# Kernel optimization log

Measured on AMD Instinct MI355X. Metric: run time of the kernel, lower is better.

Reference implementation:

```python
import jax, jax.numpy as jnp
import numpy as np

SCALE = 8.0  # sqrt(d_k), d_k = 64
NEG_INF = -1000000000.0


def setup_inputs() -> dict:
    key = jax.random.key(0)
    ks = jax.random.split(key, 7)
    B, H, S, D = 2, 8, 4096, 64
    shp = (B, H, S, D)
    q_a = jax.random.normal(ks[0], shp, dtype=jnp.float32)
    k_a = jax.random.normal(ks[1], shp, dtype=jnp.float32)
    v_a = jax.random.normal(ks[2], shp, dtype=jnp.float32)
    q_s = jax.random.normal(ks[3], shp, dtype=jnp.float32)
    k_s = jax.random.normal(ks[4], shp, dtype=jnp.float32)
    v_s = jax.random.normal(ks[5], shp, dtype=jnp.float32)
    mask = jax.random.randint(ks[6], (B, 1, 1, S), 0, 2, dtype=jnp.int32)
    return {"q_a": q_a, "k_a": k_a, "v_a": v_a,
            "q_s": q_s, "k_s": k_s, "v_s": v_s, "mask": mask}


def reference(q_a, k_a, v_a, q_s, k_s, v_s, mask):
    # a2a + a2s + s2a + s2s == (q_a + q_s) @ (k_a + k_s)^T  (exact algebra)
    q = q_a + q_s                               # [B,H,S,D]
    k = k_a + k_s                               # [B,H,S,D]
    score = jnp.einsum("bhqd,bhkd->bhqk", q, k) / SCALE  # [B,H,S,S]
    score = jnp.where(mask == 0, NEG_INF, score)
    attn = jax.nn.softmax(score, axis=-1)       # dropout p=0 (eval/identity)
    out = jnp.einsum("bhqk,bhkd->bhqd", attn, v_a + v_s)
    return out
```

## Files before the change

### kernel.cpp

```cpp
#include <hip/hip_runtime.h>
#include <hip/hip_bf16.h>

#define S_   4096
#define D_   64
#define BH_  16
#define QW   64
#define QBLK 256
#define KVB  128
#define NCH  2

typedef __attribute__((ext_vector_type(8)))  short short8_t;
typedef __attribute__((ext_vector_type(16))) float f32x16;
#define QSCALE 0.18033688011112042f

__device__ __forceinline__ unsigned short f2bf(float f) {
  unsigned u = __float_as_uint(f);
  u += 0x7fffu + ((u >> 16) & 1u);
  return (unsigned short)(u >> 16);
}

__device__ __forceinline__ void glds16(const unsigned short* g, unsigned short* l) {
  __builtin_amdgcn_global_load_lds(
      (const __attribute__((address_space(1))) unsigned int*)g,
      (__attribute__((address_space(3))) unsigned int*)l, 16, 0, 0);
}

__global__ void addcvt2_kernel(const float* __restrict__ a, const float* __restrict__ b,
                               unsigned short* __restrict__ o, float scale, int n) {
  int i = (blockIdx.x * blockDim.x + threadIdx.x) * 4;
  if (i >= n) return;
  float4 x = *(const float4*)(a + i);
  float4 y = *(const float4*)(b + i);
  ushort4 r;
  r.x = f2bf((x.x + y.x) * scale); r.y = f2bf((x.y + y.y) * scale);
  r.z = f2bf((x.z + y.z) * scale); r.w = f2bf((x.w + y.w) * scale);
  *(ushort4*)(o + i) = r;
}

__global__ void compact_kernel(const int* __restrict__ mask, int* __restrict__ idx,
                               int* __restrict__ cnt) {
  __shared__ int ps[256];
  int b = blockIdx.x, tid = threadIdx.x;
  const int* mb = mask + (size_t)b * S_;
  int m[16], c = 0;
  int base = tid * 16;
#pragma unroll
  for (int i = 0; i < 16; ++i) { m[i] = mb[base + i]; c += (m[i] != 0); }
  ps[tid] = c;
  __syncthreads();
  for (int off = 1; off < 256; off <<= 1) {
    int add = (tid >= off) ? ps[tid - off] : 0;
    __syncthreads();
    ps[tid] += add;
    __syncthreads();
  }
  int pos = ps[tid] - c;
#pragma unroll
  for (int i = 0; i < 16; ++i) if (m[i]) idx[(size_t)b * S_ + pos++] = base + i;
  if (tid == 255) cnt[b] = ps[255];
}

__global__ void kgather_kernel(const float* __restrict__ ka, const float* __restrict__ ks,
                               const int* __restrict__ idx, const int* __restrict__ cnt,
                               unsigned short* __restrict__ khat) {
  int gid = blockIdx.x * 256 + threadIdx.x;
  int e = gid * 8;
  int bh = e >> 18;
  int rem = e & 262143;
  int j = rem >> 6, d = rem & 63;
  int b = bh >> 3;
  int C = cnt[b];
  unsigned short* o = khat + (size_t)e;
  ushort4 r0 = {0, 0, 0, 0}, r1 = {0, 0, 0, 0};
  if (j < C) {
    int src = idx[(size_t)b * S_ + j];
    const float* pa = ka + ((size_t)bh * S_ + src) * D_ + d;
    const float* pb = ks + ((size_t)bh * S_ + src) * D_ + d;
    float4 x0 = *(const float4*)pa, x1 = *(const float4*)(pa + 4);
    float4 y0 = *(const float4*)pb, y1 = *(const float4*)(pb + 4);
    r0.x = f2bf(x0.x + y0.x); r0.y = f2bf(x0.y + y0.y);
    r0.z = f2bf(x0.z + y0.z); r0.w = f2bf(x0.w + y0.w);
    r1.x = f2bf(x1.x + y1.x); r1.y = f2bf(x1.y + y1.y);
    r1.z = f2bf(x1.z + y1.z); r1.w = f2bf(x1.w + y1.w);
  }
  *(ushort4*)o = r0;
  *(ushort4*)(o + 4) = r1;
}

__global__ void vgather_kernel(const float* __restrict__ va, const float* __restrict__ vs,
                               const int* __restrict__ idx, const int* __restrict__ cnt,
                               unsigned short* __restrict__ vt) {
  __shared__ __align__(16) unsigned short t[D_][72];
  int bh = blockIdx.y, b = bh >> 3;
  int s0 = blockIdx.x * 64;
  int C = cnt[b];
  int tid = threadIdx.x;
  int row16 = tid >> 4;
  int col4  = (tid & 15) * 4;
#pragma unroll
  for (int p = 0; p < 4; ++p) {
    int srow = p * 16 + row16;
    int j = s0 + srow;
    float4 x = {0, 0, 0, 0}, y = {0, 0, 0, 0};
    if (j < C) {
      int src = idx[(size_t)b * S_ + j];
      x = *(const float4*)(va + ((size_t)bh * S_ + src) * D_ + col4);
      y = *(const float4*)(vs + ((size_t)bh * S_ + src) * D_ + col4);
    }
    t[col4 + 0][srow] = f2bf(x.x + y.x);
    t[col4 + 1][srow] = f2bf(x.y + y.y);
    t[col4 + 2][srow] = f2bf(x.z + y.z);
    t[col4 + 3][srow] = f2bf(x.w + y.w);
  }
  __syncthreads();
#pragma unroll
  for (int r = 0; r < 2; ++r) {
    int e = (r * 256 + tid) * 8;
    int d = e >> 6, sc = e & 63;
    short8_t v = *(const short8_t*)&t[d][sc];
    *(short8_t*)(vt + ((size_t)bh * D_ + d) * S_ + s0 + sc) = v;
  }
}

__global__ __launch_bounds__(256, 2) void attn_kernel(
    const unsigned short* __restrict__ Qb, const unsigned short* __restrict__ Kb,
    const unsigned short* __restrict__ Vt, const int* __restrict__ cnt,
    float* __restrict__ out, float* __restrict__ Opar, float2* __restrict__ Ml) {
  __shared__ __align__(16) unsigned short lK[2][KVB * 64];
  __shared__ __align__(16) unsigned short lV[2][64 * KVB];

  const int tid  = threadIdx.x;
  const int wave = tid >> 6;
  const int lane = tid & 63;
  const int l31  = lane & 31;
  const int h5   = lane >> 5;
  const int rsw  = l31 & 7;
  const int bh   = blockIdx.y;
  const int ch   = blockIdx.z;
  const int qrow0 = blockIdx.x * QBLK + wave * QW + l31;
  const int b    = bh >> 3;
  const int C    = cnt[b];
  const int NTt  = (C + KVB - 1) / KVB;
  const int tpc  = (NTt + NCH - 1) / NCH;
  const int ts   = ch * tpc;
  const int te   = (ts + tpc < NTt) ? (ts + tpc) : NTt;

  short8_t qf[2][4];
#pragma unroll
  for (int qb = 0; qb < 2; ++qb) {
    const unsigned short* qp = Qb + ((size_t)bh * S_ + qrow0 + 32 * qb) * D_ + h5 * 8;
#pragma unroll
    for (int t4 = 0; t4 < 4; ++t4) qf[qb][t4] = *(const short8_t*)(qp + t4 * 16);
  }

  const unsigned short* gk0 = Kb + (size_t)bh * S_ * D_;
  const unsigned short* gv0 = Vt + (size_t)bh * D_ * S_;

  int srcK[4], srcV[4], ldsB[4];
#pragma unroll
  for (int r2 = 0; r2 < 4; ++r2) {
    int c = r2 * 256 + tid;
    int rowK = c >> 3, gK = (c & 7) ^ (rowK & 7);
    srcK[r2] = rowK * 64 + gK * 8;
    int rowV = c >> 4, gg = c & 15;
    int swg = (gg & 8) | ((gg & 7) ^ (rowV & 7));
    srcV[r2] = rowV * S_ + swg * 8;
    ldsB[r2] = r2 * 2048 + wave * 512;
  }

  f32x16 acc0[2], acc1[2];
  float mrow[2], lrow[2];
#pragma unroll
  for (int qb = 0; qb < 2; ++qb) {
    acc0[qb] = (f32x16)(0.0f); acc1[qb] = (f32x16)(0.0f);
    mrow[qb] = -1e30f; lrow[qb] = 0.0f;
  }

  if (ts < te) {
#pragma unroll
    for (int r2 = 0; r2 < 4; ++r2) {
      glds16(gk0 + (size_t)ts * KVB * D_ + srcK[r2], &lK[0][ldsB[r2]]);
      glds16(gv0 + ts * KVB + srcV[r2], &lV[0][ldsB[r2]]);
    }
    __syncthreads();

    for (int t = ts; t < te; ++t) {
      const int cur = (t - ts) & 1;
      if (t + 1 < te) {
#pragma unroll
        for (int r2 = 0; r2 < 4; ++r2) {
          glds16(gk0 + (size_t)(t + 1) * KVB * D_ + srcK[r2], &lK[cur ^ 1][ldsB[r2]]);
          glds16(gv0 + (t + 1) * KVB + srcV[r2], &lV[cur ^ 1][ldsB[r2]]);
        }
      }

#pragma unroll
      for (int h = 0; h < 2; ++h) {
        f32x16 sv0[2], sv1[2];
#pragma unroll
        for (int qb = 0; qb < 2; ++qb) { sv0[qb] = (f32x16)(0.0f); sv1[qb] = (f32x16)(0.0f); }
        __builtin_amdgcn_s_setprio(1);
#pragma unroll
        for (int t4 = 0; t4 < 4; ++t4) {
          int g = ((2 * t4 + h5) ^ rsw) * 8;
          short8_t kf0 = *(const short8_t*)&lK[cur][(h * 64 + l31) * 64 + g];
          short8_t kf1 = *(const short8_t*)&lK[cur][(h * 64 + 32 + l31) * 64 + g];
          sv0[0] = __builtin_amdgcn_mfma_f32_32x32x16_bf16(kf0, qf[0][t4], sv0[0], 0, 0, 0);
          sv0[1] = __builtin_amdgcn_mfma_f32_32x32x16_bf16(kf0, qf[1][t4], sv0[1], 0, 0, 0);
          sv1[0] = __builtin_amdgcn_mfma_f32_32x32x16_bf16(kf1, qf[0][t4], sv1[0], 0, 0, 0);
          sv1[1] = __builtin_amdgcn_mfma_f32_32x32x16_bf16(kf1, qf[1][t4], sv1[1], 0, 0, 0);
        }
        __builtin_amdgcn_s_setprio(0);

        if (t == NTt - 1) {
          int kvb = t * KVB + h * 64;
#pragma unroll
          for (int i = 0; i < 16; ++i) {
            int key = kvb + (i & 3) + 8 * (i >> 2) + 4 * h5;
#pragma unroll
            for (int qb = 0; qb < 2; ++qb) {
              if (key >= C) sv0[qb][i] = -1e9f;
              if (key + 32 >= C) sv1[qb][i] = -1e9f;
            }
          }
        }

        unsigned int pkw[2][16];
#pragma unroll
        for (int qb = 0; qb < 2; ++qb) {
          float tmx[8];
#pragma unroll
          for (int i = 0; i < 8; ++i)
            tmx[i] = fmaxf(fmaxf(sv0[qb][i], sv0[qb][i + 8]),
                           fmaxf(sv1[qb][i], sv1[qb][i + 8]));
#pragma unroll
          for (int i = 0; i < 4; ++i) tmx[i] = fmaxf(tmx[i], tmx[i + 4]);
          float tm = fmaxf(fmaxf(tmx[0], tmx[1]), fmaxf(tmx[2], tmx[3]));
          tm = fmaxf(tm, __shfl_xor(tm, 32));

          if (__any(tm > mrow[qb] + 8.0f)) {
            float mnew = fmaxf(mrow[qb], tm);
            float sc = __builtin_amdgcn_exp2f(mrow[qb] - mnew);
            mrow[qb] = mnew;
            lrow[qb] *= sc;
#pragma unroll
            for (int i = 0; i < 16; ++i) { acc0[qb][i] *= sc; acc1[qb][i] *= sc; }
          }

          float m = mrow[qb];
          float t0 = 0.f, t1 = 0.f, t2 = 0.f, t3 = 0.f;
#pragma unroll
          for (int i = 0; i < 16; i += 4) {
            sv0[qb][i + 0] = __builtin_amdgcn_exp2f(sv0[qb][i + 0] - m); t0 += sv0[qb][i + 0];
            sv0[qb][i + 1] = __builtin_amdgcn_exp2f(sv0[qb][i + 1] - m); t1 += sv0[qb][i + 1];
            sv0[qb][i + 2] = __builtin_amdgcn_exp2f(sv0[qb][i + 2] - m); t2 += sv0[qb][i + 2];
            sv0[qb][i + 3] = __builtin_amdgcn_exp2f(sv0[qb][i + 3] - m); t3 += sv0[qb][i + 3];
            sv1[qb][i + 0] = __builtin_amdgcn_exp2f(sv1[qb][i + 0] - m); t0 += sv1[qb][i + 0];
            sv1[qb][i + 1] = __builtin_amdgcn_exp2f(sv1[qb][i + 1] - m); t1 += sv1[qb][i + 1];
            sv1[qb][i + 2] = __builtin_amdgcn_exp2f(sv1[qb][i + 2] - m); t2 += sv1[qb][i + 2];
            sv1[qb][i + 3] = __builtin_amdgcn_exp2f(sv1[qb][i + 3] - m); t3 += sv1[qb][i + 3];
          }
          float tsum = (t0 + t1) + (t2 + t3);
          tsum += __shfl_xor(tsum, 32);
          lrow[qb] += tsum;

#pragma unroll
          for (int rg = 0; rg < 4; ++rg) {
            __hip_bfloat162 a0 = __float22bfloat162_rn({sv0[qb][rg * 4 + 0], sv0[qb][rg * 4 + 1]});
            __hip_bfloat162 a1 = __float22bfloat162_rn({sv0[qb][rg * 4 + 2], sv0[qb][rg * 4 + 3]});
            __hip_bfloat162 b0 = __float22bfloat162_rn({sv1[qb][rg * 4 + 0], sv1[qb][rg * 4 + 1]});
            __hip_bfloat162 b1 = __float22bfloat162_rn({sv1[qb][rg * 4 + 2], sv1[qb][rg * 4 + 3]});
            pkw[qb][rg * 2 + 0] = *(unsigned int*)&a0;
            pkw[qb][rg * 2 + 1] = *(unsigned int*)&a1;
            pkw[qb][8 + rg * 2 + 0] = *(unsigned int*)&b0;
            pkw[qb][8 + rg * 2 + 1] = *(unsigned int*)&b1;
          }
        }

        __builtin_amdgcn_s_setprio(1);
#pragma unroll
        for (int kt = 0; kt < 4; ++kt) {
          const int n = kt >> 1, k1 = kt & 1;
          int gcol = ((h * 8) | ((2 * kt + h5) ^ rsw)) * 8;
          short8_t vf0 = *(const short8_t*)&lV[cur][l31 * KVB + gcol];
          short8_t vf1 = *(const short8_t*)&lV[cur][(32 + l31) * KVB + gcol];
#pragma unroll
          for (int qb = 0; qb < 2; ++qb) {
            unsigned int sA = pkw[qb][n * 8 + (2 * k1 + h5) * 2 + 0];
            unsigned int sB = pkw[qb][n * 8 + (2 * k1 + h5) * 2 + 1];
            unsigned int xA = pkw[qb][n * 8 + (2 * k1 + (h5 ^ 1)) * 2 + 0];
            unsigned int xB = pkw[qb][n * 8 + (2 * k1 + (h5 ^ 1)) * 2 + 1];
            unsigned int pA = (unsigned int)__shfl_xor((int)xA, 32);
            unsigned int pB = (unsigned int)__shfl_xor((int)xB, 32);
            union { unsigned int u[4]; short8_t v; } bb;
            bb.u[0] = h5 ? pA : sA;
            bb.u[1] = h5 ? pB : sB;
            bb.u[2] = h5 ? sA : pA;
            bb.u[3] = h5 ? sB : pB;
            acc0[qb] = __builtin_amdgcn_mfma_f32_32x32x16_bf16(vf0, bb.v, acc0[qb], 0, 0, 0);
            acc1[qb] = __builtin_amdgcn_mfma_f32_32x32x16_bf16(vf1, bb.v, acc1[qb], 0, 0, 0);
          }
        }
        __builtin_amdgcn_s_setprio(0);
      }

      __syncthreads();
    }
  }

  float* Op = (ch == 0) ? out : Opar;
#pragma unroll
  for (int qb = 0; qb < 2; ++qb) {
    float* op = Op + ((size_t)bh * S_ + qrow0 + 32 * qb) * D_;
#pragma unroll
    for (int rg = 0; rg < 4; ++rg) {
      float4 o0, o1;
      o0.x = acc0[qb][rg * 4 + 0]; o0.y = acc0[qb][rg * 4 + 1];
      o0.z = acc0[qb][rg * 4 + 2]; o0.w = acc0[qb][rg * 4 + 3];
      o1.x = acc1[qb][rg * 4 + 0]; o1.y = acc1[qb][rg * 4 + 1];
      o1.z = acc1[qb][rg * 4 + 2]; o1.w = acc1[qb][rg * 4 + 3];
      *(float4*)(op + rg * 8 + h5 * 4) = o0;
      *(float4*)(op + 32 + rg * 8 + h5 * 4) = o1;
    }
    if (h5 == 0) {
      float2 st; st.x = mrow[qb]; st.y = lrow[qb];
      Ml[(size_t)ch * (BH_ * S_) + (size_t)bh * S_ + qrow0 + 32 * qb] = st;
    }
  }
}

__global__ void combine_kernel(const float* __restrict__ O1, const float2* __restrict__ Ml,
                               float* __restrict__ out) {
  int gid = blockIdx.x * 256 + threadIdx.x;
  int row = gid >> 2, qd = (gid & 3) * 16;
  float2 a = Ml[row];
  float2 b = Ml[BH_ * S_ + row];
  float M = fmaxf(a.x, b.x);
  float w0 = exp2f(a.x - M), w1 = exp2f(b.x - M);
  float inv = 1.0f / (a.y * w0 + b.y * w1);
  w0 *= inv; w1 *= inv;
  const float4* p0 = (const float4*)(out + (size_t)row * D_ + qd);
  const float4* p1 = (const float4*)(O1 + (size_t)row * D_ + qd);
  float4* po = (float4*)(out + (size_t)row * D_ + qd);
#pragma unroll
  for (int i = 0; i < 4; ++i) {
    float4 x = p0[i], y = p1[i];
    float4 r;
    r.x = x.x * w0 + y.x * w1; r.y = x.y * w0 + y.y * w1;
    r.z = x.z * w0 + y.z * w1; r.w = x.w * w0 + y.w * w1;
    po[i] = r;
  }
}

extern "C" void kernel_launch(void* const* d_in, const int* in_sizes, int n_in,
                              void* d_out, int out_size, void* d_ws, size_t ws_size,
                              hipStream_t stream) {
  const float* q_a = (const float*)d_in[0];
  const float* k_a = (const float*)d_in[1];
  const float* v_a = (const float*)d_in[2];
  const float* q_s = (const float*)d_in[3];
  const float* k_s = (const float*)d_in[4];
  const float* v_s = (const float*)d_in[5];
  const int*   mask = (const int*)d_in[6];
  float* out = (float*)d_out;
  (void)in_sizes; (void)n_in; (void)out_size; (void)ws_size;

  const int N = BH_ * S_ * D_;
  unsigned short* qb   = (unsigned short*)d_ws;
  unsigned short* khat = qb + N;
  unsigned short* vt   = khat + N;
  int*  idx  = (int*)(vt + N);
  int*  cnt  = idx + 2 * S_;
  float* O1  = (float*)(cnt + 4);
  float2* ml = (float2*)(O1 + N);

  compact_kernel<<<2, 256, 0, stream>>>(mask, idx, cnt);
  addcvt2_kernel<<<N / 1024, 256, 0, stream>>>(q_a, q_s, qb, QSCALE, N);
  kgather_kernel<<<N / 2048, 256, 0, stream>>>(k_a, k_s, idx, cnt, khat);
  {
    dim3 g(S_ / 64, BH_);
    vgather_kernel<<<g, 256, 0, stream>>>(v_a, v_s, idx, cnt, vt);
  }
  {
    dim3 g(S_ / QBLK, BH_, NCH);
    attn_kernel<<<g, 256, 0, stream>>>(qb, khat, vt, cnt, out, O1, ml);
  }
  combine_kernel<<<(BH_ * S_ * 4) / 256, 256, 0, stream>>>(O1, ml, out);
}
```

Baseline: 128.7 us.

## Fuse K and V gather kernels and interleave softmax with PV MFMAs per query block

Merges the separate K-gather and V-gather preprocessing kernels into one kernel that reads K and V rows through a single index lookup, saving one launch and a redundant idx read. It also restructures the attention inner loop so that each 32-row query block packs its P values and immediately issues its PV MFMAs, instead of packing both blocks before the MFMA phase. This is meant to shrink the live register set (pkw halves) and let the second block's exp work overlap the first block's matrix ops. The cost is a slightly different instruction schedule, plus K writes done as strided 8-byte stores from the V-transposing tile layout.

```diff
diff --git a/kernel.cpp b/kernel.cpp
--- a/kernel.cpp
+++ b/kernel.cpp
@@ -60,36 +60,11 @@
   if (tid == 255) cnt[b] = ps[255];
 }
 
-__global__ void kgather_kernel(const float* __restrict__ ka, const float* __restrict__ ks,
-                               const int* __restrict__ idx, const int* __restrict__ cnt,
-                               unsigned short* __restrict__ khat) {
-  int gid = blockIdx.x * 256 + threadIdx.x;
-  int e = gid * 8;
-  int bh = e >> 18;
-  int rem = e & 262143;
-  int j = rem >> 6, d = rem & 63;
-  int b = bh >> 3;
-  int C = cnt[b];
-  unsigned short* o = khat + (size_t)e;
-  ushort4 r0 = {0, 0, 0, 0}, r1 = {0, 0, 0, 0};
-  if (j < C) {
-    int src = idx[(size_t)b * S_ + j];
-    const float* pa = ka + ((size_t)bh * S_ + src) * D_ + d;
-    const float* pb = ks + ((size_t)bh * S_ + src) * D_ + d;
-    float4 x0 = *(const float4*)pa, x1 = *(const float4*)(pa + 4);
-    float4 y0 = *(const float4*)pb, y1 = *(const float4*)(pb + 4);
-    r0.x = f2bf(x0.x + y0.x); r0.y = f2bf(x0.y + y0.y);
-    r0.z = f2bf(x0.z + y0.z); r0.w = f2bf(x0.w + y0.w);
-    r1.x = f2bf(x1.x + y1.x); r1.y = f2bf(x1.y + y1.y);
-    r1.z = f2bf(x1.z + y1.z); r1.w = f2bf(x1.w + y1.w);
-  }
-  *(ushort4*)o = r0;
-  *(ushort4*)(o + 4) = r1;
-}
-
-__global__ void vgather_kernel(const float* __restrict__ va, const float* __restrict__ vs,
-                               const int* __restrict__ idx, const int* __restrict__ cnt,
-                               unsigned short* __restrict__ vt) {
+__global__ void kvgather_kernel(const float* __restrict__ ka, const float* __restrict__ ks,
+                                const float* __restrict__ va, const float* __restrict__ vs,
+                                const int* __restrict__ idx, const int* __restrict__ cnt,
+                                unsigned short* __restrict__ khat,
+                                unsigned short* __restrict__ vt) {
   __shared__ __align__(16) unsigned short t[D_][72];
   int bh = blockIdx.y, b = bh >> 3;
   int s0 = blockIdx.x * 64;
@@ -101,16 +76,24 @@
   for (int p = 0; p < 4; ++p) {
     int srow = p * 16 + row16;
     int j = s0 + srow;
-    float4 x = {0, 0, 0, 0}, y = {0, 0, 0, 0};
+    float4 xv = {0, 0, 0, 0}, yv = {0, 0, 0, 0};
+    float4 xk = {0, 0, 0, 0}, yk = {0, 0, 0, 0};
     if (j < C) {
       int src = idx[(size_t)b * S_ + j];
-      x = *(const float4*)(va + ((size_t)bh * S_ + src) * D_ + col4);
-      y = *(const float4*)(vs + ((size_t)bh * S_ + src) * D_ + col4);
-    }
-    t[col4 + 0][srow] = f2bf(x.x + y.x);
-    t[col4 + 1][srow] = f2bf(x.y + y.y);
-    t[col4 + 2][srow] = f2bf(x.z + y.z);
-    t[col4 + 3][srow] = f2bf(x.w + y.w);
+      size_t off = ((size_t)bh * S_ + src) * D_ + col4;
+      xv = *(const float4*)(va + off);
+      yv = *(const float4*)(vs + off);
+      xk = *(const float4*)(ka + off);
+      yk = *(const float4*)(ks + off);
+    }
+    t[col4 + 0][srow] = f2bf(xv.x + yv.x);
+    t[col4 + 1][srow] = f2bf(xv.y + yv.y);
+    t[col4 + 2][srow] = f2bf(xv.z + yv.z);
+    t[col4 + 3][srow] = f2bf(xv.w + yv.w);
+    ushort4 rk;
+    rk.x = f2bf(xk.x + yk.x); rk.y = f2bf(xk.y + yk.y);
+    rk.z = f2bf(xk.z + yk.z); rk.w = f2bf(xk.w + yk.w);
+    *(ushort4*)(khat + ((size_t)bh * S_ + j) * D_ + col4) = rk;
   }
   __syncthreads();
 #pragma unroll
@@ -225,7 +208,6 @@
           }
         }
 
-        unsigned int pkw[2][16];
 #pragma unroll
         for (int qb = 0; qb < 2; ++qb) {
           float tmx[8];
@@ -264,44 +246,49 @@
           tsum += __shfl_xor(tsum, 32);
           lrow[qb] += tsum;
 
+          unsigned int pkw[16];
 #pragma unroll
           for (int rg = 0; rg < 4; ++rg) {
             __hip_bfloat162 a0 = __float22bfloat162_rn({sv0[qb][rg * 4 + 0], sv0[qb][rg * 4 + 1]});
             __hip_bfloat162 a1 = __float22bfloat162_rn({sv0[qb][rg * 4 + 2], sv0[qb][rg * 4 + 3]});
             __hip_bfloat162 b0 = __float22bfloat162_rn({sv1[qb][rg * 4 + 0], sv1[qb][rg * 4 + 1]});
             __hip_bfloat162 b1 = __float22bfloat162_rn({sv1[qb][rg * 4 + 2], sv1[qb][rg * 4 + 3]});
-            pkw[qb][rg * 2 + 0] = *(unsigned int*)&a0;
-            pkw[qb][rg * 2 + 1] = *(unsigned int*)&a1;
-            pkw[qb][8 + rg * 2 + 0] = *(unsigned int*)&b0;
-            pkw[qb][8 + rg * 2 + 1] = *(unsigned int*)&b1;
-          }
-        }
-
-        __builtin_amdgcn_s_setprio(1);
-#pragma unroll
-        for (int kt = 0; kt < 4; ++kt) {
-          const int n = kt >> 1, k1 = kt & 1;
-          int gcol = ((h * 8) | ((2 * kt + h5) ^ rsw)) * 8;
-          short8_t vf0 = *(const short8_t*)&lV[cur][l31 * KVB + gcol];
-          short8_t vf1 = *(const short8_t*)&lV[cur][(32 + l31) * KVB + gcol];
-#pragma unroll
-          for (int qb = 0; qb < 2; ++qb) {
-            unsigned int sA = pkw[qb][n * 8 + (2 * k1 + h5) * 2 + 0];
-            unsigned int sB = pkw[qb][n * 8 + (2 * k1 + h5) * 2 + 1];
-            unsigned int xA = pkw[qb][n * 8 + (2 * k1 + (h5 ^ 1)) * 2 + 0];
-            unsigned int xB = pkw[qb][n * 8 + (2 * k1 + (h5 ^ 1)) * 2 + 1];
+            pkw[rg * 2 + 0] = *(unsigned int*)&a0;
+            pkw[rg * 2 + 1] = *(unsigned int*)&a1;
+            pkw[8 + rg * 2 + 0] = *(unsigned int*)&b0;
+            pkw[8 + rg * 2 + 1] = *(unsigned int*)&b1;
+          }
+
+          unsigned int bbu[4][4];
+#pragma unroll
+          for (int kt = 0; kt < 4; ++kt) {
+            const int n = kt >> 1, k1 = kt & 1;
+            unsigned int sA = pkw[n * 8 + (2 * k1 + h5) * 2 + 0];
+            unsigned int sB = pkw[n * 8 + (2 * k1 + h5) * 2 + 1];
+            unsigned int xA = pkw[n * 8 + (2 * k1 + (h5 ^ 1)) * 2 + 0];
+            unsigned int xB = pkw[n * 8 + (2 * k1 + (h5 ^ 1)) * 2 + 1];
             unsigned int pA = (unsigned int)__shfl_xor((int)xA, 32);
             unsigned int pB = (unsigned int)__shfl_xor((int)xB, 32);
+            bbu[kt][0] = h5 ? pA : sA;
+            bbu[kt][1] = h5 ? pB : sB;
+            bbu[kt][2] = h5 ? sA : pA;
+            bbu[kt][3] = h5 ? sB : pB;
+          }
+
+          __builtin_amdgcn_s_setprio(1);
+#pragma unroll
+          for (int kt = 0; kt < 4; ++kt) {
+            int gcol = ((h * 8) | ((2 * kt + h5) ^ rsw)) * 8;
+            short8_t vf0 = *(const short8_t*)&lV[cur][l31 * KVB + gcol];
+            short8_t vf1 = *(const short8_t*)&lV[cur][(32 + l31) * KVB + gcol];
             union { unsigned int u[4]; short8_t v; } bb;
-            bb.u[0] = h5 ? pA : sA;
-            bb.u[1] = h5 ? pB : sB;
-            bb.u[2] = h5 ? sA : pA;
-            bb.u[3] = h5 ? sB : pB;
+            bb.u[0] = bbu[kt][0]; bb.u[1] = bbu[kt][1];
+            bb.u[2] = bbu[kt][2]; bb.u[3] = bbu[kt][3];
             acc0[qb] = __builtin_amdgcn_mfma_f32_32x32x16_bf16(vf0, bb.v, acc0[qb], 0, 0, 0);
             acc1[qb] = __builtin_amdgcn_mfma_f32_32x32x16_bf16(vf1, bb.v, acc1[qb], 0, 0, 0);
           }
+          __builtin_amdgcn_s_setprio(0);
         }
-        __builtin_amdgcn_s_setprio(0);
       }
 
       __syncthreads();
@@ -376,10 +363,9 @@
 
   compact_kernel<<<2, 256, 0, stream>>>(mask, idx, cnt);
   addcvt2_kernel<<<N / 1024, 256, 0, stream>>>(q_a, q_s, qb, QSCALE, N);
-  kgather_kernel<<<N / 2048, 256, 0, stream>>>(k_a, k_s, idx, cnt, khat);
   {
     dim3 g(S_ / 64, BH_);
-    vgather_kernel<<<g, 256, 0, stream>>>(v_a, v_s, idx, cnt, vt);
+    kvgather_kernel<<<g, 256, 0, stream>>>(k_a, k_s, v_a, v_s, idx, cnt, khat, vt);
   }
   {
     dim3 g(S_ / QBLK, BH_, NCH);
```

New measurement: 139.7 us. 1.09x slower.
